# Optimization experiments

Hardware: AMD Instinct MI355X
Metric: run time of the kernel (lower is better)

## Reference

```python
import jax, jax.numpy as jnp
import numpy as np


def setup_inputs() -> dict:
    key = jax.random.key(0)
    k1, k2, k3, k4 = jax.random.split(key, 4)
    B, T, M = 4, 2048, 1024   # batch, seq, d_model -> S = 8192 tokens
    E, F = 16, 4096           # experts (world_size*num_local_experts), d_ff
    x = jax.random.normal(k1, (B, T, M), dtype=jnp.float32) * 0.02
    Wg = jax.random.normal(k2, (M, E), dtype=jnp.float32) * 0.02
    w1 = jax.random.normal(k3, (E, M, F), dtype=jnp.float32) * 0.02
    w2 = jax.random.normal(k4, (E, F, M), dtype=jnp.float32) * 0.02
    return {"x": x, "Wg": Wg, "w1": w1, "w2": w2}


def reference(x, Wg, w1, w2):
    d = x.shape[-1]
    xr = x.reshape(-1, d)                     # (S, M)
    S = xr.shape[0]
    E = Wg.shape[1]
    C = (S + E - 1) // E                      # capacity (capacity_factor = 1.0)

    # top-1 gating (gate module = linear + softmax)
    gate = jax.nn.softmax(xr @ Wg, axis=-1)   # (S, E)
    idx = jnp.argmax(gate, axis=1)            # (S,) expert index per token
    gates_s = jnp.take_along_axis(gate, idx[:, None], axis=1)[:, 0]  # (S,)

    # cumulative-sum location within chosen expert
    onehot = jax.nn.one_hot(idx, E, dtype=jnp.int32)           # (S, E)
    loc = jnp.sum((jnp.cumsum(onehot, axis=0) - 1) * onehot, axis=1)  # (S,)
    valid = loc < C                                             # capacity drop mask

    # scatter dispatch: overflow tokens routed to a pad slot C, then sliced off
    loc_pad = jnp.minimum(loc, C)
    dispatched = jnp.zeros((E, C + 1, d), dtype=x.dtype).at[idx, loc_pad].set(xr)
    dispatched = dispatched[:, :C]            # (E, C, M)

    # all-to-all is identity (FakeAllToAllOp); per-expert FFN
    h = jax.nn.relu(jnp.einsum('ecm,emf->ecf', dispatched, w1))   # (E, C, F)
    expert_out = jnp.einsum('ecf,efm->ecm', h, w2)                # (E, C, M)

    # gather combine: rout[i] = gate_s[i] * expert_out[idx[i], loc[i]] if loc < C
    gathered = expert_out[idx, jnp.minimum(loc, C - 1)]           # (S, M)
    combined = gathered * (gates_s * valid.astype(x.dtype))[:, None]
    return combined.reshape(x.shape)
```

## Files before the change

### kernel.cpp

```cpp
#include <hip/hip_runtime.h>
#include <cstdint>
#include <cstddef>

#define S_TOK 8192
#define DM    1024
#define NE    16
#define NF    4096
#define CAP   512

typedef __attribute__((ext_vector_type(8))) short bf16x8;
typedef __attribute__((ext_vector_type(4))) float f32x4;

__device__ __forceinline__ unsigned short f2bf(float f) {
  __bf16 b = (__bf16)f;
  return __builtin_bit_cast(unsigned short, b);
}
__device__ __forceinline__ unsigned pk2(float a, float b) {
  return (unsigned)f2bf(a) | ((unsigned)f2bf(b) << 16);
}
__device__ __forceinline__ int pcol(int c) { return c ^ ((c >> 3) & 7); }

__device__ __forceinline__ void gload_lds16(const void* g, void* l) {
  __builtin_amdgcn_global_load_lds(
      (const __attribute__((address_space(1))) void*)g,
      (__attribute__((address_space(3))) void*)l, 16, 0, 0);
}

__global__ void __launch_bounds__(256)
zero_kernel(float4* __restrict__ Out, int n4) {
  const int stride = gridDim.x * 256;
  for (int i = blockIdx.x * 256 + threadIdx.x; i < n4; i += stride)
    Out[i] = float4{0.f, 0.f, 0.f, 0.f};
}

__global__ void __launch_bounds__(256)
gate_kernel(const float* __restrict__ X, const float* __restrict__ Wg,
            int* __restrict__ idx, float* __restrict__ gval) {
  const int tid  = threadIdx.x;
  const int lane = tid & 63;
  const int wid  = tid >> 6;
  const int e = lane & 15, q = lane >> 4;
  const int t0 = blockIdx.x * 16 + wid * 4;
  const int mbase = q * 256;

  const float* xp0 = X + (size_t)(t0 + 0) * DM + mbase;
  const float* xp1 = X + (size_t)(t0 + 1) * DM + mbase;
  const float* xp2 = X + (size_t)(t0 + 2) * DM + mbase;
  const float* xp3 = X + (size_t)(t0 + 3) * DM + mbase;
  const float* wp  = Wg + (size_t)mbase * NE + e;

  float a0 = 0.f, a1 = 0.f, a2 = 0.f, a3 = 0.f;
#pragma unroll 4
  for (int i = 0; i < 64; ++i) {
    float4 x0 = *(const float4*)(xp0 + i * 4);
    float4 x1 = *(const float4*)(xp1 + i * 4);
    float4 x2 = *(const float4*)(xp2 + i * 4);
    float4 x3 = *(const float4*)(xp3 + i * 4);
    float w0 = wp[(i * 4 + 0) * NE];
    float w1 = wp[(i * 4 + 1) * NE];
    float w2 = wp[(i * 4 + 2) * NE];
    float w3 = wp[(i * 4 + 3) * NE];
    a0 = fmaf(x0.x, w0, fmaf(x0.y, w1, fmaf(x0.z, w2, fmaf(x0.w, w3, a0))));
    a1 = fmaf(x1.x, w0, fmaf(x1.y, w1, fmaf(x1.z, w2, fmaf(x1.w, w3, a1))));
    a2 = fmaf(x2.x, w0, fmaf(x2.y, w1, fmaf(x2.z, w2, fmaf(x2.w, w3, a2))));
    a3 = fmaf(x3.x, w0, fmaf(x3.y, w1, fmaf(x3.z, w2, fmaf(x3.w, w3, a3))));
  }
#pragma unroll
  for (int s = 16; s < 64; s <<= 1) {
    a0 += __shfl_xor(a0, s, 64);
    a1 += __shfl_xor(a1, s, 64);
    a2 += __shfl_xor(a2, s, 64);
    a3 += __shfl_xor(a3, s, 64);
  }
  float l = (q == 0) ? a0 : (q == 1) ? a1 : (q == 2) ? a2 : a3;
  float bv = l; int bi = e;
#pragma unroll
  for (int s = 1; s < 16; s <<= 1) {
    float ov = __shfl_xor(bv, s, 16);
    int   oi = __shfl_xor(bi, s, 16);
    if (ov > bv || (ov == bv && oi < bi)) { bv = ov; bi = oi; }
  }
  float p  = expf(l - bv);
  float sm = p;
#pragma unroll
  for (int s = 1; s < 16; s <<= 1) sm += __shfl_xor(sm, s, 16);
  if (e == 0) {
    idx[t0 + q]  = bi;
    gval[t0 + q] = 1.0f / sm;
  }
}

__global__ void __launch_bounds__(1024)
scan_kernel(const int* __restrict__ idx, int* __restrict__ s2t) {
  const int tid = threadIdx.x;
#pragma unroll
  for (int k = 0; k < 8; ++k) s2t[tid + k * 1024] = -1;
  __shared__ int base[16];
  __shared__ int wavecnt[16][16];
  if (tid < 16) base[tid] = 0;
  __syncthreads();
  const int wid = tid >> 6, lane = tid & 63;
  const unsigned long long ltmask = (1ull << lane) - 1ull;
  for (int c = 0; c < 8; ++c) {
    const int t = c * 1024 + tid;
    const int e = idx[t];
    int rank = 0;
#pragma unroll
    for (int ee = 0; ee < 16; ++ee) {
      unsigned long long m = __ballot(e == ee);
      if (lane == 0) wavecnt[wid][ee] = __popcll(m);
      if (ee == e) rank = __popcll(m & ltmask);
    }
    __syncthreads();
    if (tid < 16) {
      int s = base[tid];
#pragma unroll
      for (int w = 0; w < 16; ++w) { int cc = wavecnt[w][tid]; wavecnt[w][tid] = s; s += cc; }
      base[tid] = s;
    }
    __syncthreads();
    const int loc = wavecnt[wid][e] + rank;
    if (loc < CAP) s2t[e * CAP + loc] = t;
    __syncthreads();
  }
}

__global__ void __launch_bounds__(256)
gather_kernel(const float* __restrict__ X, const int* __restrict__ s2t,
              unsigned short* __restrict__ Xg) {
  const int tid = threadIdx.x;
  const int d  = tid & 127;
  const int sl = tid >> 7;
  const int s0 = blockIdx.x * 16;
#pragma unroll 2
  for (int p = 0; p < 8; ++p) {
    const int s = s0 + p * 2 + sl;
    const int tok = s2t[s];
    uint4 w;
    if (tok >= 0) {
      const float* xp = X + (size_t)tok * DM + d * 8;
      float4 v0 = *(const float4*)xp;
      float4 v1 = *(const float4*)(xp + 4);
      w = make_uint4(pk2(v0.x, v0.y), pk2(v0.z, v0.w),
                     pk2(v1.x, v1.y), pk2(v1.z, v1.w));
    } else {
      w = make_uint4(0u, 0u, 0u, 0u);
    }
    char* dst = (char*)Xg + (size_t)(s >> 9) * 1048576 +
                (size_t)(d >> 3) * 65536 + (size_t)(d & 7) * 8192 +
                (size_t)(s & 511) * 16;
    *(uint4*)dst = w;
  }
}



#define G1_BX 2
#define G1_BY 32
#define G1_BZ 16
__global__ void __launch_bounds__(512, 2)
gemm1_kernel(const unsigned short* __restrict__ Xg, const float* __restrict__ W1,
             unsigned short* __restrict__ H2) {
  constexpr int NT = DM / 64;
  __shared__ __align__(16) char lds[131072];

  const int tid = threadIdx.x;
  const int lane = tid & 63, wid = tid >> 6;
  const int wr = wid >> 1, wc = wid & 1;
  const int ln15 = lane & 15, l16 = lane >> 4;

  const int flat = blockIdx.x + G1_BX * (blockIdx.y + G1_BY * blockIdx.z);
  const int xcd = flat & 7, jj = flat >> 3;
  const int e  = xcd * 2 + (jj >> 6);
  const int rr = jj & 63;
  const int by = rr >> 1, bx = rr & 1;
  const int m0 = bx * 256, n0 = by * 128;

  char* const Bb0 = lds + 98304;
  char* const Bb1 = lds + 98304 + 16384;

  const int rb = wid >> 1;
  const int kgw = (wid & 1) * 4;
  const int adst = kgw * 4096 + rb * 1024;
  const char* const Xge = (const char*)Xg + (size_t)e * 1048576 +
                          (size_t)(m0 + rb * 64 + lane) * 16;

  const int c0 = (tid & 31) * 4;
  const int kq = tid >> 5;
  const float* const bsrc = W1 + (size_t)e * DM * NF + (size_t)(kq * 4) * NF + n0 + c0;
  const int kgb = kq >> 1, hb = kq & 1;
  int bwoff[4];
#pragma unroll
  for (int cc = 0; cc < 4; ++cc) bwoff[cc] = kgb * 2048 + pcol(c0 + cc) * 16 + hb * 8;

  int aoff[4], boff[4];
#pragma unroll
  for (int mi = 0; mi < 4; ++mi) aoff[mi] = l16 * 4096 + (wr * 64 + mi * 16 + ln15) * 16;
#pragma unroll
  for (int ni = 0; ni < 4; ++ni) boff[ni] = l16 * 2048 + pcol(wc * 64 + ni * 16 + ln15) * 16;

  f32x4 acc[4][4];
#pragma unroll
  for (int mi = 0; mi < 4; ++mi)
#pragma unroll
    for (int ni = 0; ni < 4; ++ni) acc[mi][ni] = f32x4{0.f, 0.f, 0.f, 0.f};

  float4 breg[4];

  auto ISSUE_B = [&](int kt) {
    const float* bp = bsrc + (size_t)kt * 64 * NF;
#pragma unroll
    for (int r = 0; r < 4; ++r) breg[r] = *(const float4*)(bp + (size_t)r * NF);
  };
  auto ISSUE_A = [&](int Aoff, int kt) {
#pragma unroll
    for (int j = 0; j < 4; ++j)
      gload_lds16(Xge + (size_t)kt * 65536 + (size_t)(kgw + j) * 8192,
                  lds + Aoff + adst + j * 4096);
  };
  auto WRITEB = [&](char* Bbuf) {
    const float* f = (const float*)breg;
#pragma unroll
    for (int cc = 0; cc < 4; ++cc)
      *(uint2*)(Bbuf + bwoff[cc]) =
          make_uint2(pk2(f[0 + cc], f[4 + cc]), pk2(f[8 + cc], f[12 + cc]));
  };
  auto COMPUTE = [&](int Aoff, const char* Bbuf) {
#pragma unroll
    for (int kk = 0; kk < 2; ++kk) {
      bf16x8 af[4], bf[4];
#pragma unroll
      for (int mi = 0; mi < 4; ++mi)
        af[mi] = *(const bf16x8*)(lds + Aoff + kk * 16384 + aoff[mi]);
#pragma unroll
      for (int ni = 0; ni < 4; ++ni)
        bf[ni] = *(const bf16x8*)(Bbuf + kk * 8192 + boff[ni]);
#pragma unroll
      for (int mi = 0; mi < 4; ++mi)
#pragma unroll
        for (int ni = 0; ni < 4; ++ni)
          acc[mi][ni] = __builtin_amdgcn_mfma_f32_16x16x32_bf16(af[mi], bf[ni], acc[mi][ni], 0, 0, 0);
    }
  };

  ISSUE_B(0); ISSUE_A(0, 0);
  WRITEB(Bb0);
  ISSUE_B(1); ISSUE_A(32768, 1);
  asm volatile("s_waitcnt vmcnt(8) lgkmcnt(0)" ::: "memory");
  __builtin_amdgcn_s_barrier();

  int aCur = 0, aNxt = 32768, aNx2 = 65536;
  for (int kt = 0; kt < NT; ++kt) {
    WRITEB((kt & 1) ? Bb0 : Bb1);
    const int tl = (kt + 2 < NT) ? kt + 2 : NT - 1;
    ISSUE_B(tl);
    ISSUE_A(aNx2, tl);
    COMPUTE(aCur, (kt & 1) ? Bb1 : Bb0);
    asm volatile("s_waitcnt vmcnt(8) lgkmcnt(0)" ::: "memory");
    __builtin_amdgcn_s_barrier();
    const int t = aCur; aCur = aNxt; aNxt = aNx2; aNx2 = t;
  }
  asm volatile("s_waitcnt vmcnt(0)" ::: "memory");
  __builtin_amdgcn_s_barrier();

  char* img = lds;
#pragma unroll
  for (int mi = 0; mi < 4; ++mi) {
#pragma unroll
    for (int ni = 0; ni < 4; ++ni) {
      const int colL = wc * 64 + ni * 16 + ln15;
      const int basei = (colL >> 6) * 32768 + ((colL >> 3) & 7) * 4096 + (colL & 7) * 2;
#pragma unroll
      for (int j = 0; j < 4; ++j) {
        const int rowL = wr * 64 + mi * 16 + l16 * 4 + j;
        float v = acc[mi][ni][j];
        v = v > 0.f ? v : 0.f;
        *(unsigned short*)(img + basei + rowL * 16) = f2bf(v);
      }
    }
  }
  __syncthreads();
  const char* src = img + tid * 128;
  char* dst = (char*)H2 + (size_t)e * 4194304 +
              (size_t)((n0 >> 6) + (tid >> 8)) * 65536 +
              (size_t)((tid >> 5) & 7) * 8192 +
              (size_t)(m0 + (tid & 31) * 8) * 16;
#pragma unroll
  for (int u = 0; u < 8; ++u)
    *(uint4*)(dst + u * 16) = *(const uint4*)(src + u * 16);
}

#define G2_BX 2
#define G2_BY 8
#define G2_BZ 16
__global__ void __launch_bounds__(512, 2)
gemm2_kernel(const unsigned short* __restrict__ H2, const float* __restrict__ W2,
             const int* __restrict__ s2t, const float* __restrict__ gval,
             float* __restrict__ Out) {
  constexpr int NT = NF / 64;
  __shared__ __align__(16) char lds[131072];

  const int tid = threadIdx.x;
  const int lane = tid & 63, wid = tid >> 6;
  const int wr = wid >> 1, wc = wid & 1;
  const int ln15 = lane & 15, l16 = lane >> 4;

  const int flat = blockIdx.x + G2_BX * (blockIdx.y + G2_BY * blockIdx.z);
  const int xcd = flat & 7, jj = flat >> 3;
  const int e  = xcd * 2 + (jj >> 4);
  const int rr = jj & 15;
  const int by = rr >> 1, bx = rr & 1;
  const int m0 = bx * 256, n0 = by * 128;

  char* const Bb0 = lds + 98304;
  char* const Bb1 = lds + 98304 + 16384;

  const int rb = wid >> 1;
  const int kgw = (wid & 1) * 4;
  const int adst = kgw * 4096 + rb * 1024;
  const char* const Hex = (const char*)H2 + (size_t)e * 4194304 + (size_t)m0 * 16 +
                          (size_t)(rb * 64 + lane) * 16;

  const int c0 = (tid & 31) * 4;
  const int kq = tid >> 5;
  const float* const bsrc = W2 + (size_t)e * NF * DM + (size_t)(kq * 4) * DM + n0 + c0;
  const int kgb = kq >> 1, hb = kq & 1;
  int bwoff[4];
#pragma unroll
  for (int cc = 0; cc < 4; ++cc) bwoff[cc] = kgb * 2048 + pcol(c0 + cc) * 16 + hb * 8;

  int aoff[4], boff[4];
#pragma unroll
  for (int mi = 0; mi < 4; ++mi) aoff[mi] = l16 * 4096 + (wr * 64 + mi * 16 + ln15) * 16;
#pragma unroll
  for (int ni = 0; ni < 4; ++ni) boff[ni] = l16 * 2048 + pcol(wc * 64 + ni * 16 + ln15) * 16;

  f32x4 acc[4][4];
#pragma unroll
  for (int mi = 0; mi < 4; ++mi)
#pragma unroll
    for (int ni = 0; ni < 4; ++ni) acc[mi][ni] = f32x4{0.f, 0.f, 0.f, 0.f};

  float4 breg[4];

  auto ISSUE_B = [&](int kt) {
    const float* bp = bsrc + (size_t)kt * 64 * DM;
#pragma unroll
    for (int r = 0; r < 4; ++r) breg[r] = *(const float4*)(bp + (size_t)r * DM);
  };
  auto ISSUE_A = [&](int Aoff, int kt) {
#pragma unroll
    for (int j = 0; j < 4; ++j)
      gload_lds16(Hex + (size_t)kt * 65536 + (size_t)(kgw + j) * 8192,
                  lds + Aoff + adst + j * 4096);
  };
  auto WRITEB = [&](char* Bbuf) {
    const float* f = (const float*)breg;
#pragma unroll
    for (int cc = 0; cc < 4; ++cc)
      *(uint2*)(Bbuf + bwoff[cc]) =
          make_uint2(pk2(f[0 + cc], f[4 + cc]), pk2(f[8 + cc], f[12 + cc]));
  };
  auto COMPUTE = [&](int Aoff, const char* Bbuf) {
#pragma unroll
    for (int kk = 0; kk < 2; ++kk) {
      bf16x8 af[4], bf[4];
#pragma unroll
      for (int mi = 0; mi < 4; ++mi)
        af[mi] = *(const bf16x8*)(lds + Aoff + kk * 16384 + aoff[mi]);
#pragma unroll
      for (int ni = 0; ni < 4; ++ni)
        bf[ni] = *(const bf16x8*)(Bbuf + kk * 8192 + boff[ni]);
#pragma unroll
      for (int mi = 0; mi < 4; ++mi)
#pragma unroll
        for (int ni = 0; ni < 4; ++ni)
          acc[mi][ni] = __builtin_amdgcn_mfma_f32_16x16x32_bf16(af[mi], bf[ni], acc[mi][ni], 0, 0, 0);
    }
  };

  ISSUE_B(0); ISSUE_A(0, 0);
  WRITEB(Bb0);
  ISSUE_B(1); ISSUE_A(32768, 1);
  asm volatile("s_waitcnt vmcnt(8) lgkmcnt(0)" ::: "memory");
  __builtin_amdgcn_s_barrier();

  int aCur = 0, aNxt = 32768, aNx2 = 65536;
  for (int kt = 0; kt < NT; ++kt) {
    WRITEB((kt & 1) ? Bb0 : Bb1);
    const int tl = (kt + 2 < NT) ? kt + 2 : NT - 1;
    ISSUE_B(tl);
    ISSUE_A(aNx2, tl);
    COMPUTE(aCur, (kt & 1) ? Bb1 : Bb0);
    asm volatile("s_waitcnt vmcnt(8) lgkmcnt(0)" ::: "memory");
    __builtin_amdgcn_s_barrier();
    const int t = aCur; aCur = aNxt; aNxt = aNx2; aNx2 = t;
  }
  asm volatile("s_waitcnt vmcnt(0)" ::: "memory");

#pragma unroll
  for (int mi = 0; mi < 4; ++mi) {
#pragma unroll
    for (int ni = 0; ni < 4; ++ni) {
      const int col = n0 + wc * 64 + ni * 16 + ln15;
#pragma unroll
      for (int j = 0; j < 4; ++j) {
        const int row = m0 + wr * 64 + mi * 16 + l16 * 4 + j;
        const int tk = s2t[e * CAP + row];
        if (tk >= 0)
          Out[(size_t)tk * DM + col] = acc[mi][ni][j] * gval[tk];
      }
    }
  }
}

extern "C" void kernel_launch(void* const* d_in, const int* in_sizes, int n_in,
                              void* d_out, int out_size, void* d_ws, size_t ws_size,
                              hipStream_t stream) {
  (void)in_sizes; (void)n_in; (void)ws_size;
  const float* X  = (const float*)d_in[0];
  const float* Wg = (const float*)d_in[1];
  const float* W1 = (const float*)d_in[2];
  const float* W2 = (const float*)d_in[3];
  float* Out = (float*)d_out;

  char* ws = (char*)d_ws;
  int*   s2t  = (int*)ws;
  int*   idx  = (int*)(ws + 32768);
  float* gval = (float*)(ws + 65536);
  unsigned short* Xg = (unsigned short*)(ws + 98304);
  unsigned short* H2 = (unsigned short*)(ws + 98304 + 16777216);

  zero_kernel<<<2048, 256, 0, stream>>>((float4*)Out, out_size / 4);
  gate_kernel<<<S_TOK / 16, 256, 0, stream>>>(X, Wg, idx, gval);
  scan_kernel<<<1, 1024, 0, stream>>>(idx, s2t);
  gather_kernel<<<512, 256, 0, stream>>>(X, s2t, Xg);
  gemm1_kernel<<<dim3(G1_BX, G1_BY, G1_BZ), 512, 0, stream>>>(Xg, W1, H2);
  gemm2_kernel<<<dim3(G2_BX, G2_BY, G2_BZ), 512, 0, stream>>>(H2, W2, s2t, gval, Out);
}
```

Baseline: 280.2 us.

## Deepen W prefetch to two register sets and raise MFMA wave priority

Both expert GEMM kernels now keep two register buffers for the fp32 weight tile, so global loads for B run three k-steps ahead instead of two. The main loop is unrolled by two with fixed LDS buffers, and tail prefetch indices wrap with a mask instead of clamping. The MFMA block is also wrapped in s_setprio so compute waves get issue priority. This aims to hide more global-load latency of the fp32 weights, at the cost of extra VGPRs, which could hurt occupancy under the 512x2 launch bounds, plus a few redundant wrapped loads at the end.

```diff
diff --git a/kernel.cpp b/kernel.cpp
--- a/kernel.cpp
+++ b/kernel.cpp
@@ -162,6 +162,7 @@
 gemm1_kernel(const unsigned short* __restrict__ Xg, const float* __restrict__ W1,
              unsigned short* __restrict__ H2) {
   constexpr int NT = DM / 64;
+  constexpr int NTM = NT - 1;
   __shared__ __align__(16) char lds[131072];
 
   const int tid = threadIdx.x;
@@ -182,8 +183,8 @@
   const int rb = wid >> 1;
   const int kgw = (wid & 1) * 4;
   const int adst = kgw * 4096 + rb * 1024;
-  const char* const Xge = (const char*)Xg + (size_t)e * 1048576 +
-                          (size_t)(m0 + rb * 64 + lane) * 16;
+  const char* const aSrc = (const char*)Xg + (size_t)e * 1048576 +
+                           (size_t)(m0 + rb * 64 + lane) * 16;
 
   const int c0 = (tid & 31) * 4;
   const int kq = tid >> 5;
@@ -205,21 +206,21 @@
 #pragma unroll
     for (int ni = 0; ni < 4; ++ni) acc[mi][ni] = f32x4{0.f, 0.f, 0.f, 0.f};
 
-  float4 breg[4];
-
-  auto ISSUE_B = [&](int kt) {
+  float4 bA[4], bB[4];
+
+  auto ISSUE_B = [&](float4* br, int kt) {
     const float* bp = bsrc + (size_t)kt * 64 * NF;
 #pragma unroll
-    for (int r = 0; r < 4; ++r) breg[r] = *(const float4*)(bp + (size_t)r * NF);
+    for (int r = 0; r < 4; ++r) br[r] = *(const float4*)(bp + (size_t)r * NF);
   };
   auto ISSUE_A = [&](int Aoff, int kt) {
 #pragma unroll
     for (int j = 0; j < 4; ++j)
-      gload_lds16(Xge + (size_t)kt * 65536 + (size_t)(kgw + j) * 8192,
+      gload_lds16(aSrc + (size_t)kt * 65536 + (size_t)(kgw + j) * 8192,
                   lds + Aoff + adst + j * 4096);
   };
-  auto WRITEB = [&](char* Bbuf) {
-    const float* f = (const float*)breg;
+  auto WRITEB = [&](char* Bbuf, const float4* br) {
+    const float* f = (const float*)br;
 #pragma unroll
     for (int cc = 0; cc < 4; ++cc)
       *(uint2*)(Bbuf + bwoff[cc]) =
@@ -235,30 +236,40 @@
 #pragma unroll
       for (int ni = 0; ni < 4; ++ni)
         bf[ni] = *(const bf16x8*)(Bbuf + kk * 8192 + boff[ni]);
+      __builtin_amdgcn_s_setprio(1);
 #pragma unroll
       for (int mi = 0; mi < 4; ++mi)
 #pragma unroll
         for (int ni = 0; ni < 4; ++ni)
           acc[mi][ni] = __builtin_amdgcn_mfma_f32_16x16x32_bf16(af[mi], bf[ni], acc[mi][ni], 0, 0, 0);
-    }
-  };
-
-  ISSUE_B(0); ISSUE_A(0, 0);
-  WRITEB(Bb0);
-  ISSUE_B(1); ISSUE_A(32768, 1);
-  asm volatile("s_waitcnt vmcnt(8) lgkmcnt(0)" ::: "memory");
+      __builtin_amdgcn_s_setprio(0);
+    }
+  };
+
+  ISSUE_B(bA, 0); ISSUE_A(0, 0);
+  WRITEB(Bb0, bA);
+  ISSUE_B(bB, 1); ISSUE_A(32768, 1);
+  ISSUE_B(bA, 2);
+  asm volatile("s_waitcnt vmcnt(12) lgkmcnt(0)" ::: "memory");
   __builtin_amdgcn_s_barrier();
 
   int aCur = 0, aNxt = 32768, aNx2 = 65536;
-  for (int kt = 0; kt < NT; ++kt) {
-    WRITEB((kt & 1) ? Bb0 : Bb1);
-    const int tl = (kt + 2 < NT) ? kt + 2 : NT - 1;
-    ISSUE_B(tl);
-    ISSUE_A(aNx2, tl);
-    COMPUTE(aCur, (kt & 1) ? Bb1 : Bb0);
+#pragma unroll 1
+  for (int kt = 0; kt < NT; kt += 2) {
+    WRITEB(Bb1, bB);
+    ISSUE_B(bB, (kt + 3) & NTM);
+    ISSUE_A(aNx2, (kt + 2) & NTM);
+    COMPUTE(aCur, Bb0);
     asm volatile("s_waitcnt vmcnt(8) lgkmcnt(0)" ::: "memory");
     __builtin_amdgcn_s_barrier();
-    const int t = aCur; aCur = aNxt; aNxt = aNx2; aNx2 = t;
+    int t = aCur; aCur = aNxt; aNxt = aNx2; aNx2 = t;
+    WRITEB(Bb0, bA);
+    ISSUE_B(bA, (kt + 4) & NTM);
+    ISSUE_A(aNx2, (kt + 3) & NTM);
+    COMPUTE(aCur, Bb1);
+    asm volatile("s_waitcnt vmcnt(8) lgkmcnt(0)" ::: "memory");
+    __builtin_amdgcn_s_barrier();
+    t = aCur; aCur = aNxt; aNxt = aNx2; aNx2 = t;
   }
   asm volatile("s_waitcnt vmcnt(0)" ::: "memory");
   __builtin_amdgcn_s_barrier();
@@ -298,6 +309,7 @@
              const int* __restrict__ s2t, const float* __restrict__ gval,
              float* __restrict__ Out) {
   constexpr int NT = NF / 64;
+  constexpr int NTM = NT - 1;
   __shared__ __align__(16) char lds[131072];
 
   const int tid = threadIdx.x;
@@ -318,8 +330,8 @@
   const int rb = wid >> 1;
   const int kgw = (wid & 1) * 4;
   const int adst = kgw * 4096 + rb * 1024;
-  const char* const Hex = (const char*)H2 + (size_t)e * 4194304 + (size_t)m0 * 16 +
-                          (size_t)(rb * 64 + lane) * 16;
+  const char* const aSrc = (const char*)H2 + (size_t)e * 4194304 +
+                           (size_t)(m0 + rb * 64 + lane) * 16;
 
   const int c0 = (tid & 31) * 4;
   const int kq = tid >> 5;
@@ -341,21 +353,21 @@
 #pragma unroll
     for (int ni = 0; ni < 4; ++ni) acc[mi][ni] = f32x4{0.f, 0.f, 0.f, 0.f};
 
-  float4 breg[4];
-
-  auto ISSUE_B = [&](int kt) {
+  float4 bA[4], bB[4];
+
+  auto ISSUE_B = [&](float4* br, int kt) {
     const float* bp = bsrc + (size_t)kt * 64 * DM;
 #pragma unroll
-    for (int r = 0; r < 4; ++r) breg[r] = *(const float4*)(bp + (size_t)r * DM);
+    for (int r = 0; r < 4; ++r) br[r] = *(const float4*)(bp + (size_t)r * DM);
   };
   auto ISSUE_A = [&](int Aoff, int kt) {
 #pragma unroll
     for (int j = 0; j < 4; ++j)
-      gload_lds16(Hex + (size_t)kt * 65536 + (size_t)(kgw + j) * 8192,
+      gload_lds16(aSrc + (size_t)kt * 65536 + (size_t)(kgw + j) * 8192,
                   lds + Aoff + adst + j * 4096);
   };
-  auto WRITEB = [&](char* Bbuf) {
-    const float* f = (const float*)breg;
+  auto WRITEB = [&](char* Bbuf, const float4* br) {
+    const float* f = (const float*)br;
 #pragma unroll
     for (int cc = 0; cc < 4; ++cc)
       *(uint2*)(Bbuf + bwoff[cc]) =
@@ -371,30 +383,40 @@
 #pragma unroll
       for (int ni = 0; ni < 4; ++ni)
         bf[ni] = *(const bf16x8*)(Bbuf + kk * 8192 + boff[ni]);
+      __builtin_amdgcn_s_setprio(1);
 #pragma unroll
       for (int mi = 0; mi < 4; ++mi)
 #pragma unroll
         for (int ni = 0; ni < 4; ++ni)
           acc[mi][ni] = __builtin_amdgcn_mfma_f32_16x16x32_bf16(af[mi], bf[ni], acc[mi][ni], 0, 0, 0);
-    }
-  };
-
-  ISSUE_B(0); ISSUE_A(0, 0);
-  WRITEB(Bb0);
-  ISSUE_B(1); ISSUE_A(32768, 1);
-  asm volatile("s_waitcnt vmcnt(8) lgkmcnt(0)" ::: "memory");
+      __builtin_amdgcn_s_setprio(0);
+    }
+  };
+
+  ISSUE_B(bA, 0); ISSUE_A(0, 0);
+  WRITEB(Bb0, bA);
+  ISSUE_B(bB, 1); ISSUE_A(32768, 1);
+  ISSUE_B(bA, 2);
+  asm volatile("s_waitcnt vmcnt(12) lgkmcnt(0)" ::: "memory");
   __builtin_amdgcn_s_barrier();
 
   int aCur = 0, aNxt = 32768, aNx2 = 65536;
-  for (int kt = 0; kt < NT; ++kt) {
-    WRITEB((kt & 1) ? Bb0 : Bb1);
-    const int tl = (kt + 2 < NT) ? kt + 2 : NT - 1;
-    ISSUE_B(tl);
-    ISSUE_A(aNx2, tl);
-    COMPUTE(aCur, (kt & 1) ? Bb1 : Bb0);
+#pragma unroll 1
+  for (int kt = 0; kt < NT; kt += 2) {
+    WRITEB(Bb1, bB);
+    ISSUE_B(bB, (kt + 3) & NTM);
+    ISSUE_A(aNx2, (kt + 2) & NTM);
+    COMPUTE(aCur, Bb0);
     asm volatile("s_waitcnt vmcnt(8) lgkmcnt(0)" ::: "memory");
     __builtin_amdgcn_s_barrier();
-    const int t = aCur; aCur = aNxt; aNxt = aNx2; aNx2 = t;
+    int t = aCur; aCur = aNxt; aNxt = aNx2; aNx2 = t;
+    WRITEB(Bb0, bA);
+    ISSUE_B(bA, (kt + 4) & NTM);
+    ISSUE_A(aNx2, (kt + 3) & NTM);
+    COMPUTE(aCur, Bb1);
+    asm volatile("s_waitcnt vmcnt(8) lgkmcnt(0)" ::: "memory");
+    __builtin_amdgcn_s_barrier();
+    t = aCur; aCur = aNxt; aNxt = aNx2; aNx2 = t;
   }
   asm volatile("s_waitcnt vmcnt(0)" ::: "memory");
 
```

Measured after the change: 284.8 us. No clear change (+1.6%).
